# Performance work log

Hardware: AMD Instinct MI355X
Metric: run time of the kernel (lower is better)

The kernel has to match this reference:

```python
import jax, jax.numpy as jnp
import numpy as np

NUM_HEADS = 8
NUM_GROUPS = 32
EPS = 1e-4


def group_norm(x, scale, bias):
    # x: [b, L, C]; normalize over (L, channels-within-group) per flax GroupNorm
    b, l, c = x.shape
    xg = x.reshape(b, l, NUM_GROUPS, c // NUM_GROUPS)
    mean = jnp.mean(xg, axis=(1, 3), keepdims=True)
    var = jnp.var(xg, axis=(1, 3), keepdims=True)
    xg = (xg - mean) * jax.lax.rsqrt(var + EPS)
    return xg.reshape(b, l, c) * scale + bias


def setup_inputs() -> dict:
    key = jax.random.key(0)
    ks = jax.random.split(key, 6)
    bs, L, C = 4, 1024, 512
    hf = C // NUM_HEADS  # 64
    x = jax.random.normal(ks[0], (bs, L, C), dtype=jnp.float32)
    W_qkv = jax.random.normal(ks[1], (C, C * 2), dtype=jnp.float32) * (1.0 / C)
    gn_qkv_scale = jnp.ones((C * 2,), dtype=jnp.float32)
    gn_qkv_bias = jnp.zeros((C * 2,), dtype=jnp.float32)
    rel_emb = jax.random.normal(ks[2], (hf * 2, 2 * L - 1), dtype=jnp.float32) * (1.0 / hf)
    gn_out_scale = jnp.ones((C,), dtype=jnp.float32)
    gn_out_bias = jnp.zeros((C,), dtype=jnp.float32)
    return {
        "x": x,
        "W_qkv": W_qkv,
        "gn_qkv_scale": gn_qkv_scale,
        "gn_qkv_bias": gn_qkv_bias,
        "rel_emb": rel_emb,
        "gn_out_scale": gn_out_scale,
        "gn_out_bias": gn_out_bias,
    }


def reference(x, W_qkv, gn_qkv_scale, gn_qkv_bias, rel_emb, gn_out_scale, gn_out_bias):
    bs, L, C = x.shape
    hf = C // NUM_HEADS
    qkv = x @ W_qkv                                # [b, L, 2C]
    qkv = group_norm(qkv, gn_qkv_scale, gn_qkv_bias)
    qkv = qkv.reshape(bs, L, NUM_HEADS, hf * 2).transpose((0, 2, 3, 1))  # [b,h,2hf,L]
    q = qkv[:, :, : hf // 2]          # [b,h,hf/2,L]
    k = qkv[:, :, hf // 2: hf]        # [b,h,hf/2,L]
    v = qkv[:, :, hf:]                # [b,h,hf,L]
    # relative distance index: rel[i,j] = i - j + L - 1
    rel_idx = jnp.arange(L)[:, None] - jnp.arange(L)[None, :] + (L - 1)
    rpe = rel_emb[:, rel_idx]         # [2hf, L, L]
    rpe_q = rpe[: hf // 2]
    rpe_k = rpe[hf // 2: hf]
    rpe_v = rpe[hf:]
    logits = (
        jnp.einsum('bhdi,bhdj->bhij', q, k)
        + jnp.einsum('bhdi,dij->bhij', q, rpe_k)
        + jnp.einsum('bhdi,dij->bhij', k, rpe_q)
    )
    attn = jax.nn.softmax(logits, axis=3).astype(jnp.float32)
    wv = jnp.einsum('bhij,bhdj->bhdi', attn, v)
    wve = jnp.einsum('bhij,dij->bhdi', attn, rpe_v)
    out = (wv + wve).transpose((0, 3, 1, 2)).reshape(bs, L, C)
    return group_norm(out, gn_out_scale, gn_out_bias)
```

## Files before the change

### kernel.cpp

```cpp
#include <hip/hip_runtime.h>
#include <hip/hip_bf16.h>

typedef unsigned short ushort;
typedef __attribute__((ext_vector_type(8))) short bf16x8;
typedef __attribute__((ext_vector_type(4))) float f32x4;
typedef __attribute__((ext_vector_type(4))) unsigned short ushort4v;

#define BSZ  4
#define LSEQ 1024
#define CIN  512
#define C2   1024
#define NH   8
#define GEPS 1e-4f

static __device__ __forceinline__ ushort f2b(float f) {
    __hip_bfloat16 h = __float2bfloat16(f);
    return *reinterpret_cast<ushort*>(&h);
}
static __device__ __forceinline__ float b2f(ushort u) {
    __hip_bfloat16 h = *reinterpret_cast<__hip_bfloat16*>(&u);
    return __bfloat162float(h);
}

__global__ __launch_bounds__(256) void prep_xsplit(const float* __restrict__ x,
                                                   ushort* __restrict__ xh,
                                                   ushort* __restrict__ xl) {
    const size_t i4 = (size_t)blockIdx.x * 256 + threadIdx.x;
    const float4 v = *reinterpret_cast<const float4*>(&x[i4 * 4]);
    ushort4v h, lo;
    const float vv[4] = {v.x, v.y, v.z, v.w};
    #pragma unroll
    for (int c = 0; c < 4; ++c) {
        const ushort hh = f2b(vv[c]);
        h[c] = hh;
        lo[c] = f2b(vv[c] - b2f(hh));
    }
    *reinterpret_cast<ushort4v*>(&xh[i4 * 4]) = h;
    *reinterpret_cast<ushort4v*>(&xl[i4 * 4]) = lo;
}

__global__ __launch_bounds__(256) void prep_wT(const float* __restrict__ W,
                                               ushort* __restrict__ wth,
                                               ushort* __restrict__ wtl) {
    __shared__ float tl[64][65];
    const int k0 = blockIdx.y * 64, n0 = blockIdx.x * 64;
    const int t = threadIdx.x;
    #pragma unroll
    for (int u = 0; u < 16; ++u) {
        const int idx = t + 256 * u;
        const int kk = idx >> 6, nn = idx & 63;
        tl[kk][nn] = W[(size_t)(k0 + kk) * 1024 + n0 + nn];
    }
    __syncthreads();
    #pragma unroll
    for (int u = 0; u < 16; ++u) {
        const int idx = t + 256 * u;
        const int nn = idx >> 6, kk = idx & 63;
        const float v = tl[kk][nn];
        const ushort h = f2b(v);
        wth[(size_t)(n0 + nn) * 512 + k0 + kk] = h;
        wtl[(size_t)(n0 + nn) * 512 + k0 + kk] = f2b(v - b2f(h));
    }
}

__global__ __launch_bounds__(256) void prep_rel(const float* __restrict__ rel,
                                                ushort* __restrict__ relT,
                                                ushort* __restrict__ relV) {
    const int t = threadIdx.x;
    if (blockIdx.x < 32) {
        __shared__ float tl[64][65];
        const int r0 = blockIdx.x * 64;
        #pragma unroll
        for (int u = 0; u < 16; ++u) {
            const int idx = t + 256 * u;
            const int dd = idx >> 6, rr = idx & 63;
            int r = r0 + rr; if (r > 2046) r = 2046;
            tl[dd][rr] = rel[(size_t)(dd ^ 32) * 2047 + r];
        }
        __syncthreads();
        #pragma unroll
        for (int u = 0; u < 16; ++u) {
            const int idx = t + 256 * u;
            const int rr = idx >> 6, dd = idx & 63;
            relT[(size_t)(r0 + rr) * 64 + dd] = f2b(tl[dd][rr]);
        }
    } else {
        const int idx = (blockIdx.x - 32) * 256 + t;
        const int dv = idx >> 11, r = idx & 2047;
        const int rc = r > 2046 ? 2046 : r;
        relV[(size_t)dv * 2048 + r] = f2b(rel[(size_t)(64 + dv) * 2047 + rc]);
    }
}

__global__ __launch_bounds__(256) void gemm_qkv_mfma(const ushort* __restrict__ xh,
                                                     const ushort* __restrict__ xl,
                                                     const ushort* __restrict__ wth,
                                                     const ushort* __restrict__ wtl,
                                                     float* __restrict__ qkv,
                                                     float* __restrict__ sumq) {
    __shared__ ushort Ah[128][40];
    __shared__ ushort Al[128][40];
    __shared__ ushort Bh[128][40];
    __shared__ ushort Bl[128][40];
    const int t = threadIdx.x;
    const int w = t >> 6, l = t & 63;
    const int lr = l & 15, lq = l >> 4;
    const int wm = w >> 1, wn = w & 1;
    const int m0 = blockIdx.y * 128, n0 = blockIdx.x * 128;
    const int b = m0 >> 10;
    f32x4 acc[4][4] = {};
    for (int k0 = 0; k0 < 512; k0 += 32) {
        __syncthreads();
        #pragma unroll
        for (int u = 0; u < 2; ++u) {
            const int idx = t + 256 * u;
            const int r = idx >> 2, c16 = (idx & 3) * 8;
            *(bf16x8*)&Ah[r][c16] = *(const bf16x8*)&xh[(size_t)(m0 + r) * 512 + k0 + c16];
            *(bf16x8*)&Al[r][c16] = *(const bf16x8*)&xl[(size_t)(m0 + r) * 512 + k0 + c16];
            *(bf16x8*)&Bh[r][c16] = *(const bf16x8*)&wth[(size_t)(n0 + r) * 512 + k0 + c16];
            *(bf16x8*)&Bl[r][c16] = *(const bf16x8*)&wtl[(size_t)(n0 + r) * 512 + k0 + c16];
        }
        __syncthreads();
        bf16x8 ah[4], av[4];
        #pragma unroll
        for (int mi = 0; mi < 4; ++mi) {
            ah[mi] = *(const bf16x8*)&Ah[64 * wm + 16 * mi + lr][8 * lq];
            av[mi] = *(const bf16x8*)&Al[64 * wm + 16 * mi + lr][8 * lq];
        }
        #pragma unroll
        for (int ni = 0; ni < 4; ++ni) {
            const bf16x8 bh = *(const bf16x8*)&Bh[64 * wn + 16 * ni + lr][8 * lq];
            const bf16x8 bl = *(const bf16x8*)&Bl[64 * wn + 16 * ni + lr][8 * lq];
            #pragma unroll
            for (int mi = 0; mi < 4; ++mi) {
                f32x4 a = acc[mi][ni];
                a = __builtin_amdgcn_mfma_f32_16x16x32_bf16(ah[mi], bl, a, 0, 0, 0);
                a = __builtin_amdgcn_mfma_f32_16x16x32_bf16(av[mi], bh, a, 0, 0, 0);
                a = __builtin_amdgcn_mfma_f32_16x16x32_bf16(ah[mi], bh, a, 0, 0, 0);
                acc[mi][ni] = a;
            }
        }
    }
    #pragma unroll
    for (int mi = 0; mi < 4; ++mi)
        #pragma unroll
        for (int ni = 0; ni < 4; ++ni)
            #pragma unroll
            for (int e = 0; e < 4; ++e)
                qkv[(size_t)(m0 + 64 * wm + 16 * mi + 4 * lq + e) * 1024 + n0 + 64 * wn + 16 * ni + lr] = acc[mi][ni][e];
    #pragma unroll
    for (int ni = 0; ni < 4; ++ni) {
        float s = 0.f, s2 = 0.f;
        #pragma unroll
        for (int mi = 0; mi < 4; ++mi)
            #pragma unroll
            for (int e = 0; e < 4; ++e) { const float v = acc[mi][ni][e]; s += v; s2 += v * v; }
        #pragma unroll
        for (int o = 32; o; o >>= 1) { s += __shfl_xor(s, o, 64); s2 += __shfl_xor(s2, o, 64); }
        if (l == 0) {
            const int g = (n0 + 64 * wn + 16 * ni) >> 5;
            atomicAdd(&sumq[(b * 32 + g) * 2 + 0], s);
            atomicAdd(&sumq[(b * 32 + g) * 2 + 1], s2);
        }
    }
}

__global__ __launch_bounds__(256) void gn_apply_bf(const float* __restrict__ qkv,
                                                   const float* __restrict__ sumq,
                                                   const float* __restrict__ scale,
                                                   const float* __restrict__ bias,
                                                   ushort* __restrict__ qg,
                                                   ushort* __restrict__ qlo,
                                                   ushort* __restrict__ vb) {
    __shared__ float tile[64][65];
    const int b  = blockIdx.z;
    const int l0 = blockIdx.y * 64, c0 = blockIdx.x * 64;
    const int t  = threadIdx.x;
    const bool vhalf = (c0 & 64);
    const int h = c0 >> 7;
    #pragma unroll
    for (int u = 0; u < 16; ++u) {
        const int idx = t + 256 * u;
        const int lr = idx >> 6, cr = idx & 63;
        const int c = c0 + cr, g = c >> 5;
        const float s  = sumq[(b * 32 + g) * 2 + 0];
        const float s2 = sumq[(b * 32 + g) * 2 + 1];
        const float mu = s * (1.f / 32768.f);
        const float rr = rsqrtf(fmaxf(s2 * (1.f / 32768.f) - mu * mu, 0.f) + GEPS);
        float v = qkv[(size_t)(b * LSEQ + l0 + lr) * C2 + c];
        v = (v - mu) * rr * scale[c] + bias[c];
        const ushort hi = f2b(v);
        qg[(size_t)(b * LSEQ + l0 + lr) * C2 + c] = hi;
        if (vhalf) tile[lr][cr] = v;
        else qlo[(size_t)(b * LSEQ + l0 + lr) * 512 + h * 64 + cr] = f2b(v - b2f(hi));
    }
    if (vhalf) {
        __syncthreads();
        #pragma unroll
        for (int u = 0; u < 16; ++u) {
            const int idx = t + 256 * u;
            const int cw = idx >> 6, lw = idx & 63;
            vb[((size_t)((b * NH + h) * 64 + cw)) * LSEQ + l0 + lw] = f2b(tile[lw][cw]);
        }
    }
}

__global__ __launch_bounds__(256) void attn_mfma(const ushort* __restrict__ qg,
                                                 const ushort* __restrict__ qlo,
                                                 const ushort* __restrict__ vbuf,
                                                 const ushort* __restrict__ relT,
                                                 const ushort* __restrict__ relV,
                                                 float* __restrict__ aout,
                                                 float* __restrict__ sumo) {
    __shared__ __align__(16) ushort rT[128][72];
    __shared__ __align__(16) ushort rV[64][136];
    __shared__ __align__(16) ushort vj[64][72];
    __shared__ __align__(16) ushort TUb[4][16][88];
    __shared__ __align__(16) ushort Ps[4][16][72];
    __shared__ __align__(16) ushort Pr[4][16][104];

    const int t = threadIdx.x;
    const int w = t >> 6, l = t & 63;
    const int lr = l & 15, lq = l >> 4;
    const int i0 = blockIdx.x * 64;
    const int h = blockIdx.y, b = blockIdx.z;
    const int ck0 = w >> 1;

    const size_t arow = (size_t)(b * LSEQ + i0 + 16 * w + lr);
    const bf16x8 a_q  = *(const bf16x8*)&qg[arow * C2 + h * 128 + 8 * lq];
    const bf16x8 a_k  = *(const bf16x8*)&qg[arow * C2 + h * 128 + 32 + 8 * lq];
    const bf16x8 a_ql = *(const bf16x8*)&qlo[arow * 512 + h * 64 + 8 * lq];

    {
        uint* pz = (uint*)&Pr[w][0][0];
        #pragma unroll
        for (int u = 0; u < 13; ++u) pz[l + 64 * u] = 0;
    }

    float m_r[4], l_r[4];
    #pragma unroll
    for (int e = 0; e < 4; ++e) { m_r[e] = -3.0e38f; l_r[e] = 0.f; }
    f32x4 Oa[4] = {};

    const size_t vbase = (size_t)((b * NH + h) * 64) * LSEQ;
    const int tbase = 4 * lq + 63 - lr;
    const int prbase = 16 * w - 32 * ck0 + 63 + 4 * lq - lr;

    for (int j0 = 0; j0 < LSEQ; j0 += 64) {
        const int r0 = i0 - j0 + 960;
        __syncthreads();
        #pragma unroll
        for (int u = 0; u < 4; ++u) {
            const int idx = t + 256 * u;
            const int rl = idx >> 3, c8 = (idx & 7) * 8;
            *(bf16x8*)&rT[rl][c8] = *(const bf16x8*)&relT[(size_t)(r0 + rl) * 64 + c8];
        }
        #pragma unroll
        for (int u = 0; u < 4; ++u) {
            const int idx = t + 256 * u;
            const int dv = idx >> 4, c8 = (idx & 15) * 8;
            *(bf16x8*)&rV[dv][c8] = *(const bf16x8*)&relV[(size_t)dv * 2048 + r0 + c8];
        }
        #pragma unroll
        for (int u = 0; u < 2; ++u) {
            const int idx = t + 256 * u;
            const int dv = idx >> 3, c8 = (idx & 7) * 8;
            *(bf16x8*)&vj[dv][c8] = *(const bf16x8*)&vbuf[vbase + (size_t)dv * LSEQ + j0 + c8];
        }
        __syncthreads();

        #pragma unroll
        for (int ct5 = 0; ct5 < 5; ++ct5) {
            const int rr = 16 * (w + ct5) + lr;
            f32x4 acc = {0.f, 0.f, 0.f, 0.f};
            acc = __builtin_amdgcn_mfma_f32_16x16x32_bf16(a_q, *(const bf16x8*)&rT[rr][8 * lq], acc, 0, 0, 0);
            acc = __builtin_amdgcn_mfma_f32_16x16x32_bf16(a_k, *(const bf16x8*)&rT[rr][32 + 8 * lq], acc, 0, 0, 0);
            #pragma unroll
            for (int e = 0; e < 4; ++e) TUb[w][4 * lq + e][16 * ct5 + lr] = f2b(acc[e]);
        }

        f32x4 sv[4];
        #pragma unroll
        for (int n = 0; n < 4; ++n) {
            const size_t krow = (size_t)(b * LSEQ + j0 + 16 * n + lr);
            const bf16x8 b_hi = *(const bf16x8*)&qg[krow * C2 + h * 128 + 32 + 8 * lq];
            const bf16x8 b_lo = *(const bf16x8*)&qlo[krow * 512 + h * 64 + 32 + 8 * lq];
            f32x4 acc = {0.f, 0.f, 0.f, 0.f};
            acc = __builtin_amdgcn_mfma_f32_16x16x32_bf16(a_q,  b_lo, acc, 0, 0, 0);
            acc = __builtin_amdgcn_mfma_f32_16x16x32_bf16(a_ql, b_hi, acc, 0, 0, 0);
            acc = __builtin_amdgcn_mfma_f32_16x16x32_bf16(a_q,  b_hi, acc, 0, 0, 0);
            #pragma unroll
            for (int e = 0; e < 4; ++e) acc[e] += b2f(TUb[w][4 * lq + e][tbase + e - 16 * n]);
            sv[n] = acc;
        }

        float mx[4];
        #pragma unroll
        for (int e = 0; e < 4; ++e)
            mx[e] = fmaxf(fmaxf(sv[0][e], sv[1][e]), fmaxf(sv[2][e], sv[3][e]));
        #pragma unroll
        for (int o = 1; o < 16; o <<= 1)
            #pragma unroll
            for (int e = 0; e < 4; ++e) mx[e] = fmaxf(mx[e], __shfl_xor(mx[e], o, 64));
        float alpha[4], ssum[4];
        #pragma unroll
        for (int e = 0; e < 4; ++e) {
            const float mn = fmaxf(m_r[e], mx[e]);
            alpha[e] = __expf(m_r[e] - mn);
            m_r[e] = mn;
            ssum[e] = 0.f;
        }
        #pragma unroll
        for (int n = 0; n < 4; ++n)
            #pragma unroll
            for (int e = 0; e < 4; ++e) {
                const float p = __expf(sv[n][e] - m_r[e]);
                ssum[e] += p;
                const ushort pb = f2b(p);
                Ps[w][4 * lq + e][16 * n + lr] = pb;
                Pr[w][4 * lq + e][prbase + e - 16 * n] = pb;
            }
        #pragma unroll
        for (int o = 1; o < 16; o <<= 1)
            #pragma unroll
            for (int e = 0; e < 4; ++e) ssum[e] += __shfl_xor(ssum[e], o, 64);
        #pragma unroll
        for (int e = 0; e < 4; ++e) l_r[e] = l_r[e] * alpha[e] + ssum[e];

        const bf16x8 pa0 = *(const bf16x8*)&Ps[w][lr][8 * lq];
        const bf16x8 pa1 = *(const bf16x8*)&Ps[w][lr][32 + 8 * lq];
        bf16x8 pra[3];
        #pragma unroll
        for (int kk = 0; kk < 3; ++kk) pra[kk] = *(const bf16x8*)&Pr[w][lr][32 * kk + 8 * lq];
        #pragma unroll
        for (int n = 0; n < 4; ++n) {
            f32x4 acc = Oa[n];
            #pragma unroll
            for (int e = 0; e < 4; ++e) acc[e] *= alpha[e];
            acc = __builtin_amdgcn_mfma_f32_16x16x32_bf16(pa0, *(const bf16x8*)&vj[16 * n + lr][8 * lq], acc, 0, 0, 0);
            acc = __builtin_amdgcn_mfma_f32_16x16x32_bf16(pa1, *(const bf16x8*)&vj[16 * n + lr][32 + 8 * lq], acc, 0, 0, 0);
            #pragma unroll
            for (int kk = 0; kk < 3; ++kk) {
                const bf16x8 brv = *(const bf16x8*)&rV[16 * n + lr][32 * (ck0 + kk) + 8 * lq];
                acc = __builtin_amdgcn_mfma_f32_16x16x32_bf16(pra[kk], brv, acc, 0, 0, 0);
            }
            Oa[n] = acc;
        }
    }

    #pragma unroll
    for (int n = 0; n < 4; ++n) {
        float s = 0.f, s2 = 0.f;
        #pragma unroll
        for (int e = 0; e < 4; ++e) {
            const float o = Oa[n][e] / l_r[e];
            aout[((size_t)(b * LSEQ + i0 + 16 * w + 4 * lq + e)) * CIN + h * 64 + 16 * n + lr] = o;
            s += o; s2 += o * o;
        }
        #pragma unroll
        for (int o = 32; o; o >>= 1) { s += __shfl_xor(s, o, 64); s2 += __shfl_xor(s2, o, 64); }
        if (l == 0) {
            atomicAdd(&sumo[(b * 32 + h * 4 + n) * 2 + 0], s);
            atomicAdd(&sumo[(b * 32 + h * 4 + n) * 2 + 1], s2);
        }
    }
}

__global__ __launch_bounds__(256) void gn_out_apply(const float* __restrict__ aout,
                                                    const float* __restrict__ sumo,
                                                    const float* __restrict__ scale,
                                                    const float* __restrict__ bias,
                                                    float* __restrict__ out) {
    const int idx4 = blockIdx.x * 256 + threadIdx.x;
    const int c = (idx4 & 127) * 4;
    const size_t row = idx4 >> 7;
    const int b = (int)(row >> 10);
    const int g = c >> 4;
    const float s  = sumo[(b * 32 + g) * 2 + 0];
    const float s2 = sumo[(b * 32 + g) * 2 + 1];
    const float mu = s * (1.f / 16384.f);
    const float rr = rsqrtf(fmaxf(s2 * (1.f / 16384.f) - mu * mu, 0.f) + GEPS);
    const float4 v = *reinterpret_cast<const float4*>(&aout[row * 512 + c]);
    const float4 sc = *reinterpret_cast<const float4*>(&scale[c]);
    const float4 bi = *reinterpret_cast<const float4*>(&bias[c]);
    float4 o;
    o.x = (v.x - mu) * rr * sc.x + bi.x;
    o.y = (v.y - mu) * rr * sc.y + bi.y;
    o.z = (v.z - mu) * rr * sc.z + bi.z;
    o.w = (v.w - mu) * rr * sc.w + bi.w;
    *reinterpret_cast<float4*>(&out[row * 512 + c]) = o;
}

extern "C" void kernel_launch(void* const* d_in, const int* in_sizes, int n_in,
                              void* d_out, int out_size, void* d_ws, size_t ws_size,
                              hipStream_t stream) {
    (void)in_sizes; (void)n_in; (void)out_size; (void)ws_size;
    const float* x   = (const float*)d_in[0];
    const float* W   = (const float*)d_in[1];
    const float* gqs = (const float*)d_in[2];
    const float* gqb = (const float*)d_in[3];
    const float* rel = (const float*)d_in[4];
    const float* gos = (const float*)d_in[5];
    const float* gob = (const float*)d_in[6];
    float* out = (float*)d_out;

    char* ws = (char*)d_ws;
    float*  qkv  = (float*)ws;
    ushort* qg   = (ushort*)(ws + (16u << 20));
    ushort* vb   = (ushort*)(ws + (24u << 20));
    ushort* rTb  = (ushort*)(ws + (28u << 20));
    ushort* rVb  = (ushort*)(ws + (28u << 20) + (256u << 10));
    ushort* qlo  = (ushort*)(ws + (28u << 20) + (512u << 10));
    float*  aout = (float*)ws;
    float*  stats = (float*)(ws + (32u << 20) + (512u << 10));
    float* sumq = stats;
    float* sumo = stats + 256;
    ushort* xhi = (ushort*)(ws + (16u << 20));
    ushort* xlo = (ushort*)(ws + (20u << 20));
    ushort* wth = (ushort*)(ws + (24u << 20));
    ushort* wtl = (ushort*)(ws + (25u << 20));

    hipMemsetAsync(stats, 0, 2048, stream);
    prep_xsplit<<<2048, 256, 0, stream>>>(x, xhi, xlo);
    prep_wT<<<dim3(16, 8), 256, 0, stream>>>(W, wth, wtl);
    prep_rel<<<544, 256, 0, stream>>>(rel, rTb, rVb);
    gemm_qkv_mfma<<<dim3(8, 32), 256, 0, stream>>>(xhi, xlo, wth, wtl, qkv, sumq);
    gn_apply_bf<<<dim3(16, 16, BSZ), 256, 0, stream>>>(qkv, sumq, gqs, gqb, qg, qlo, vb);
    attn_mfma<<<dim3(16, NH, BSZ), 256, 0, stream>>>(qg, qlo, vb, rTb, rVb, aout, sumo);
    gn_out_apply<<<2048, 256, 0, stream>>>(aout, sumo, gos, gob, out);
}
```

Before: 231.9 us.

## Fuse prep kernels, use direct global-to-LDS loads with XOR swizzle, remap grids

Merges the three preprocessing kernels into one launch. The QKV GEMM and the attention kernel now load tiles with global_load_lds (16-byte direct-to-LDS) into unpadded, XOR-swizzled shared arrays. The GEMM tile shrinks to 128x64 so it launches 512 workgroups, and both kernels use a 1D grid with an XCD-aware block remap. The attention kernel also hoists the K operand loads ahead of the barrier and shares one LDS buffer between the TU and P stages. The aim is to cut launch overhead, VGPR staging of loads and LDS bank conflicts, and to raise occupancy and L2 locality, at the cost of more complex indexing.

```diff
diff --git a/kernel.cpp b/kernel.cpp
--- a/kernel.cpp
+++ b/kernel.cpp
@@ -2,6 +2,7 @@
 #include <hip/hip_bf16.h>
 
 typedef unsigned short ushort;
+typedef unsigned int uint;
 typedef __attribute__((ext_vector_type(8))) short bf16x8;
 typedef __attribute__((ext_vector_type(4))) float f32x4;
 typedef __attribute__((ext_vector_type(4))) unsigned short ushort4v;
@@ -22,73 +23,79 @@
     return __bfloat162float(h);
 }
 
-__global__ __launch_bounds__(256) void prep_xsplit(const float* __restrict__ x,
-                                                   ushort* __restrict__ xh,
-                                                   ushort* __restrict__ xl) {
-    const size_t i4 = (size_t)blockIdx.x * 256 + threadIdx.x;
-    const float4 v = *reinterpret_cast<const float4*>(&x[i4 * 4]);
-    ushort4v h, lo;
-    const float vv[4] = {v.x, v.y, v.z, v.w};
-    #pragma unroll
-    for (int c = 0; c < 4; ++c) {
-        const ushort hh = f2b(vv[c]);
-        h[c] = hh;
-        lo[c] = f2b(vv[c] - b2f(hh));
-    }
-    *reinterpret_cast<ushort4v*>(&xh[i4 * 4]) = h;
-    *reinterpret_cast<ushort4v*>(&xl[i4 * 4]) = lo;
-}
-
-__global__ __launch_bounds__(256) void prep_wT(const float* __restrict__ W,
-                                               ushort* __restrict__ wth,
-                                               ushort* __restrict__ wtl) {
-    __shared__ float tl[64][65];
-    const int k0 = blockIdx.y * 64, n0 = blockIdx.x * 64;
-    const int t = threadIdx.x;
-    #pragma unroll
-    for (int u = 0; u < 16; ++u) {
-        const int idx = t + 256 * u;
-        const int kk = idx >> 6, nn = idx & 63;
-        tl[kk][nn] = W[(size_t)(k0 + kk) * 1024 + n0 + nn];
-    }
-    __syncthreads();
-    #pragma unroll
-    for (int u = 0; u < 16; ++u) {
-        const int idx = t + 256 * u;
-        const int nn = idx >> 6, kk = idx & 63;
-        const float v = tl[kk][nn];
-        const ushort h = f2b(v);
-        wth[(size_t)(n0 + nn) * 512 + k0 + kk] = h;
-        wtl[(size_t)(n0 + nn) * 512 + k0 + kk] = f2b(v - b2f(h));
-    }
-}
-
-__global__ __launch_bounds__(256) void prep_rel(const float* __restrict__ rel,
+static __device__ __forceinline__ void gl16(const void* g, void* l) {
+    __builtin_amdgcn_global_load_lds((const __attribute__((address_space(1))) void*)g,
+                                     (__attribute__((address_space(3))) void*)l, 16, 0, 0);
+}
+
+__global__ __launch_bounds__(256) void prep_all(const float* __restrict__ x,
+                                                const float* __restrict__ W,
+                                                const float* __restrict__ rel,
+                                                ushort* __restrict__ xh,
+                                                ushort* __restrict__ xl,
+                                                ushort* __restrict__ wth,
+                                                ushort* __restrict__ wtl,
                                                 ushort* __restrict__ relT,
                                                 ushort* __restrict__ relV) {
+    __shared__ float tl[64][65];
     const int t = threadIdx.x;
-    if (blockIdx.x < 32) {
-        __shared__ float tl[64][65];
-        const int r0 = blockIdx.x * 64;
+    const int bid = blockIdx.x;
+    if (bid < 2048) {
+        const size_t i4 = (size_t)bid * 256 + t;
+        const float4 v = *reinterpret_cast<const float4*>(&x[i4 * 4]);
+        ushort4v h, lo;
+        const float vv[4] = {v.x, v.y, v.z, v.w};
+        #pragma unroll
+        for (int c = 0; c < 4; ++c) {
+            const ushort hh = f2b(vv[c]);
+            h[c] = hh;
+            lo[c] = f2b(vv[c] - b2f(hh));
+        }
+        *reinterpret_cast<ushort4v*>(&xh[i4 * 4]) = h;
+        *reinterpret_cast<ushort4v*>(&xl[i4 * 4]) = lo;
+    } else if (bid < 2176) {
+        const int bb = bid - 2048;
+        const int k0 = (bb >> 4) * 64, n0 = (bb & 15) * 64;
         #pragma unroll
         for (int u = 0; u < 16; ++u) {
             const int idx = t + 256 * u;
-            const int dd = idx >> 6, rr = idx & 63;
-            int r = r0 + rr; if (r > 2046) r = 2046;
-            tl[dd][rr] = rel[(size_t)(dd ^ 32) * 2047 + r];
+            const int kk = idx >> 6, nn = idx & 63;
+            tl[kk][nn] = W[(size_t)(k0 + kk) * 1024 + n0 + nn];
         }
         __syncthreads();
         #pragma unroll
         for (int u = 0; u < 16; ++u) {
             const int idx = t + 256 * u;
-            const int rr = idx >> 6, dd = idx & 63;
-            relT[(size_t)(r0 + rr) * 64 + dd] = f2b(tl[dd][rr]);
+            const int nn = idx >> 6, kk = idx & 63;
+            const float v = tl[kk][nn];
+            const ushort h = f2b(v);
+            wth[(size_t)(n0 + nn) * 512 + k0 + kk] = h;
+            wtl[(size_t)(n0 + nn) * 512 + k0 + kk] = f2b(v - b2f(h));
         }
     } else {
-        const int idx = (blockIdx.x - 32) * 256 + t;
-        const int dv = idx >> 11, r = idx & 2047;
-        const int rc = r > 2046 ? 2046 : r;
-        relV[(size_t)dv * 2048 + r] = f2b(rel[(size_t)(64 + dv) * 2047 + rc]);
+        const int bb = bid - 2176;
+        if (bb < 32) {
+            const int r0 = bb * 64;
+            #pragma unroll
+            for (int u = 0; u < 16; ++u) {
+                const int idx = t + 256 * u;
+                const int dd = idx >> 6, rr = idx & 63;
+                int r = r0 + rr; if (r > 2046) r = 2046;
+                tl[dd][rr] = rel[(size_t)(dd ^ 32) * 2047 + r];
+            }
+            __syncthreads();
+            #pragma unroll
+            for (int u = 0; u < 16; ++u) {
+                const int idx = t + 256 * u;
+                const int rr = idx >> 6, dd = idx & 63;
+                relT[(size_t)(r0 + rr) * 64 + dd] = f2b(tl[dd][rr]);
+            }
+        } else {
+            const int idx = (bb - 32) * 256 + t;
+            const int dv = idx >> 11, r = idx & 2047;
+            const int rc = r > 2046 ? 2046 : r;
+            relV[(size_t)dv * 2048 + r] = f2b(rel[(size_t)(64 + dv) * 2047 + rc]);
+        }
     }
 }
 
@@ -98,41 +105,55 @@
                                                      const ushort* __restrict__ wtl,
                                                      float* __restrict__ qkv,
                                                      float* __restrict__ sumq) {
-    __shared__ ushort Ah[128][40];
-    __shared__ ushort Al[128][40];
-    __shared__ ushort Bh[128][40];
-    __shared__ ushort Bl[128][40];
+    __shared__ ushort Ah[128][32];
+    __shared__ ushort Al[128][32];
+    __shared__ ushort Bh[64][32];
+    __shared__ ushort Bl[64][32];
     const int t = threadIdx.x;
     const int w = t >> 6, l = t & 63;
     const int lr = l & 15, lq = l >> 4;
-    const int wm = w >> 1, wn = w & 1;
-    const int m0 = blockIdx.y * 128, n0 = blockIdx.x * 128;
+    const int wg = blockIdx.x;
+    const int lg = (wg & 7) * 64 + (wg >> 3);
+    const int n0 = (lg & 15) * 64;
+    const int m0 = (lg >> 4) * 128;
     const int b = m0 >> 10;
-    f32x4 acc[4][4] = {};
+    f32x4 acc[2][4] = {};
     for (int k0 = 0; k0 < 512; k0 += 32) {
         __syncthreads();
         #pragma unroll
         for (int u = 0; u < 2; ++u) {
-            const int idx = t + 256 * u;
-            const int r = idx >> 2, c16 = (idx & 3) * 8;
-            *(bf16x8*)&Ah[r][c16] = *(const bf16x8*)&xh[(size_t)(m0 + r) * 512 + k0 + c16];
-            *(bf16x8*)&Al[r][c16] = *(const bf16x8*)&xl[(size_t)(m0 + r) * 512 + k0 + c16];
-            *(bf16x8*)&Bh[r][c16] = *(const bf16x8*)&wth[(size_t)(n0 + r) * 512 + k0 + c16];
-            *(bf16x8*)&Bl[r][c16] = *(const bf16x8*)&wtl[(size_t)(n0 + r) * 512 + k0 + c16];
-        }
-        __syncthreads();
-        bf16x8 ah[4], av[4];
-        #pragma unroll
-        for (int mi = 0; mi < 4; ++mi) {
-            ah[mi] = *(const bf16x8*)&Ah[64 * wm + 16 * mi + lr][8 * lq];
-            av[mi] = *(const bf16x8*)&Al[64 * wm + 16 * mi + lr][8 * lq];
+            const int s = (2 * w + u) * 64 + l;
+            const int row = s >> 2, pc = (s & 3) << 4;
+            const int lc = pc ^ ((row & 3) << 4);
+            const size_t src = (size_t)(m0 + row) * 512 + k0 + (lc >> 1);
+            gl16(&xh[src], (ushort*)&Ah[0][0] + (2 * w + u) * 512);
+            gl16(&xl[src], (ushort*)&Al[0][0] + (2 * w + u) * 512);
+        }
+        {
+            const int s = w * 64 + l;
+            const int row = s >> 2, pc = (s & 3) << 4;
+            const int lc = pc ^ ((row & 3) << 4);
+            const size_t src = (size_t)(n0 + row) * 512 + k0 + (lc >> 1);
+            gl16(&wth[src], (ushort*)&Bh[0][0] + w * 512);
+            gl16(&wtl[src], (ushort*)&Bl[0][0] + w * 512);
+        }
+        __syncthreads();
+        bf16x8 ah[2], av[2];
+        #pragma unroll
+        for (int mi = 0; mi < 2; ++mi) {
+            const int row = 32 * w + 16 * mi + lr;
+            const int sw = (row & 3) << 3;
+            ah[mi] = *(const bf16x8*)&Ah[row][(8 * lq) ^ sw];
+            av[mi] = *(const bf16x8*)&Al[row][(8 * lq) ^ sw];
         }
         #pragma unroll
         for (int ni = 0; ni < 4; ++ni) {
-            const bf16x8 bh = *(const bf16x8*)&Bh[64 * wn + 16 * ni + lr][8 * lq];
-            const bf16x8 bl = *(const bf16x8*)&Bl[64 * wn + 16 * ni + lr][8 * lq];
-            #pragma unroll
-            for (int mi = 0; mi < 4; ++mi) {
+            const int rowb = 16 * ni + lr;
+            const int swb = (rowb & 3) << 3;
+            const bf16x8 bh = *(const bf16x8*)&Bh[rowb][(8 * lq) ^ swb];
+            const bf16x8 bl = *(const bf16x8*)&Bl[rowb][(8 * lq) ^ swb];
+            #pragma unroll
+            for (int mi = 0; mi < 2; ++mi) {
                 f32x4 a = acc[mi][ni];
                 a = __builtin_amdgcn_mfma_f32_16x16x32_bf16(ah[mi], bl, a, 0, 0, 0);
                 a = __builtin_amdgcn_mfma_f32_16x16x32_bf16(av[mi], bh, a, 0, 0, 0);
@@ -142,23 +163,23 @@
         }
     }
     #pragma unroll
-    for (int mi = 0; mi < 4; ++mi)
+    for (int mi = 0; mi < 2; ++mi)
         #pragma unroll
         for (int ni = 0; ni < 4; ++ni)
             #pragma unroll
             for (int e = 0; e < 4; ++e)
-                qkv[(size_t)(m0 + 64 * wm + 16 * mi + 4 * lq + e) * 1024 + n0 + 64 * wn + 16 * ni + lr] = acc[mi][ni][e];
+                qkv[(size_t)(m0 + 32 * w + 16 * mi + 4 * lq + e) * 1024 + n0 + 16 * ni + lr] = acc[mi][ni][e];
     #pragma unroll
     for (int ni = 0; ni < 4; ++ni) {
         float s = 0.f, s2 = 0.f;
         #pragma unroll
-        for (int mi = 0; mi < 4; ++mi)
+        for (int mi = 0; mi < 2; ++mi)
             #pragma unroll
             for (int e = 0; e < 4; ++e) { const float v = acc[mi][ni][e]; s += v; s2 += v * v; }
         #pragma unroll
         for (int o = 32; o; o >>= 1) { s += __shfl_xor(s, o, 64); s2 += __shfl_xor(s2, o, 64); }
         if (l == 0) {
-            const int g = (n0 + 64 * wn + 16 * ni) >> 5;
+            const int g = (n0 + 16 * ni) >> 5;
             atomicAdd(&sumq[(b * 32 + g) * 2 + 0], s);
             atomicAdd(&sumq[(b * 32 + g) * 2 + 1], s2);
         }
@@ -212,18 +233,19 @@
                                                  const ushort* __restrict__ relV,
                                                  float* __restrict__ aout,
                                                  float* __restrict__ sumo) {
-    __shared__ __align__(16) ushort rT[128][72];
-    __shared__ __align__(16) ushort rV[64][136];
-    __shared__ __align__(16) ushort vj[64][72];
-    __shared__ __align__(16) ushort TUb[4][16][88];
-    __shared__ __align__(16) ushort Ps[4][16][72];
-    __shared__ __align__(16) ushort Pr[4][16][104];
+    __shared__ ushort rT[128][64];
+    __shared__ ushort rV[64][128];
+    __shared__ ushort vj[64][64];
+    __shared__ ushort sA[4][16][88];
+    __shared__ ushort sPr[4][16][104];
 
     const int t = threadIdx.x;
     const int w = t >> 6, l = t & 63;
     const int lr = l & 15, lq = l >> 4;
-    const int i0 = blockIdx.x * 64;
-    const int h = blockIdx.y, b = blockIdx.z;
+    const int wg = blockIdx.x;
+    const int lg = (wg & 7) * 64 + (wg >> 3);
+    const int ib = lg & 15, h = (lg >> 4) & 7, b = lg >> 7;
+    const int i0 = ib * 64;
     const int ck0 = w >> 1;
 
     const size_t arow = (size_t)(b * LSEQ + i0 + 16 * w + lr);
@@ -232,7 +254,7 @@
     const bf16x8 a_ql = *(const bf16x8*)&qlo[arow * 512 + h * 64 + 8 * lq];
 
     {
-        uint* pz = (uint*)&Pr[w][0][0];
+        uint* pz = (uint*)&sPr[w][0][0];
         #pragma unroll
         for (int u = 0; u < 13; ++u) pz[l + 64 * u] = 0;
     }
@@ -243,54 +265,64 @@
     f32x4 Oa[4] = {};
 
     const size_t vbase = (size_t)((b * NH + h) * 64) * LSEQ;
-    const int tbase = 4 * lq + 63 - lr;
+    const int tb = 4 * lq + 63 - lr;
     const int prbase = 16 * w - 32 * ck0 + 63 + 4 * lq - lr;
 
     for (int j0 = 0; j0 < LSEQ; j0 += 64) {
         const int r0 = i0 - j0 + 960;
+
+        bf16x8 kb_hi[4], kb_lo[4];
+        #pragma unroll
+        for (int n = 0; n < 4; ++n) {
+            const size_t krow = (size_t)(b * LSEQ + j0 + 16 * n + lr);
+            kb_hi[n] = *(const bf16x8*)&qg[krow * C2 + h * 128 + 32 + 8 * lq];
+            kb_lo[n] = *(const bf16x8*)&qlo[krow * 512 + h * 64 + 32 + 8 * lq];
+        }
+
         __syncthreads();
         #pragma unroll
         for (int u = 0; u < 4; ++u) {
-            const int idx = t + 256 * u;
-            const int rl = idx >> 3, c8 = (idx & 7) * 8;
-            *(bf16x8*)&rT[rl][c8] = *(const bf16x8*)&relT[(size_t)(r0 + rl) * 64 + c8];
+            const int s = (4 * w + u) * 64 + l;
+            const int row = s >> 3, pc = (s & 7) << 4;
+            const int lc = pc ^ ((row & 7) << 4);
+            gl16(&relT[(size_t)(r0 + row) * 64 + (lc >> 1)], (ushort*)&rT[0][0] + (4 * w + u) * 512);
         }
         #pragma unroll
         for (int u = 0; u < 4; ++u) {
-            const int idx = t + 256 * u;
-            const int dv = idx >> 4, c8 = (idx & 15) * 8;
-            *(bf16x8*)&rV[dv][c8] = *(const bf16x8*)&relV[(size_t)dv * 2048 + r0 + c8];
+            const int s = (4 * w + u) * 64 + l;
+            const int row = s >> 4, pc = (s & 15) << 4;
+            const int lc = pc ^ ((row & 7) << 4);
+            gl16(&relV[(size_t)row * 2048 + r0 + (lc >> 1)], (ushort*)&rV[0][0] + (4 * w + u) * 512);
         }
         #pragma unroll
         for (int u = 0; u < 2; ++u) {
-            const int idx = t + 256 * u;
-            const int dv = idx >> 3, c8 = (idx & 7) * 8;
-            *(bf16x8*)&vj[dv][c8] = *(const bf16x8*)&vbuf[vbase + (size_t)dv * LSEQ + j0 + c8];
+            const int s = (2 * w + u) * 64 + l;
+            const int row = s >> 3, pc = (s & 7) << 4;
+            const int lc = pc ^ ((row & 7) << 4);
+            gl16(&vbuf[vbase + (size_t)row * LSEQ + j0 + (lc >> 1)], (ushort*)&vj[0][0] + (2 * w + u) * 512);
         }
         __syncthreads();
 
         #pragma unroll
         for (int ct5 = 0; ct5 < 5; ++ct5) {
             const int rr = 16 * (w + ct5) + lr;
+            const int sw = (rr & 7) << 3;
             f32x4 acc = {0.f, 0.f, 0.f, 0.f};
-            acc = __builtin_amdgcn_mfma_f32_16x16x32_bf16(a_q, *(const bf16x8*)&rT[rr][8 * lq], acc, 0, 0, 0);
-            acc = __builtin_amdgcn_mfma_f32_16x16x32_bf16(a_k, *(const bf16x8*)&rT[rr][32 + 8 * lq], acc, 0, 0, 0);
-            #pragma unroll
-            for (int e = 0; e < 4; ++e) TUb[w][4 * lq + e][16 * ct5 + lr] = f2b(acc[e]);
+            acc = __builtin_amdgcn_mfma_f32_16x16x32_bf16(a_q, *(const bf16x8*)&rT[rr][(8 * lq) ^ sw], acc, 0, 0, 0);
+            acc = __builtin_amdgcn_mfma_f32_16x16x32_bf16(a_k, *(const bf16x8*)&rT[rr][(32 + 8 * lq) ^ sw], acc, 0, 0, 0);
+            #pragma unroll
+            for (int e = 0; e < 4; ++e) sA[w][4 * lq + e][16 * ct5 + lr] = f2b(acc[e]);
         }
 
         f32x4 sv[4];
         #pragma unroll
         for (int n = 0; n < 4; ++n) {
-            const size_t krow = (size_t)(b * LSEQ + j0 + 16 * n + lr);
-            const bf16x8 b_hi = *(const bf16x8*)&qg[krow * C2 + h * 128 + 32 + 8 * lq];
-            const bf16x8 b_lo = *(const bf16x8*)&qlo[krow * 512 + h * 64 + 32 + 8 * lq];
             f32x4 acc = {0.f, 0.f, 0.f, 0.f};
-            acc = __builtin_amdgcn_mfma_f32_16x16x32_bf16(a_q,  b_lo, acc, 0, 0, 0);
-            acc = __builtin_amdgcn_mfma_f32_16x16x32_bf16(a_ql, b_hi, acc, 0, 0, 0);
-            acc = __builtin_amdgcn_mfma_f32_16x16x32_bf16(a_q,  b_hi, acc, 0, 0, 0);
-            #pragma unroll
-            for (int e = 0; e < 4; ++e) acc[e] += b2f(TUb[w][4 * lq + e][tbase + e - 16 * n]);
+            acc = __builtin_amdgcn_mfma_f32_16x16x32_bf16(a_q,  kb_lo[n], acc, 0, 0, 0);
+            acc = __builtin_amdgcn_mfma_f32_16x16x32_bf16(a_ql, kb_hi[n], acc, 0, 0, 0);
+            acc = __builtin_amdgcn_mfma_f32_16x16x32_bf16(a_q,  kb_hi[n], acc, 0, 0, 0);
+            #pragma unroll
+            for (int e = 0; e < 4; ++e) acc[e] += b2f(sA[w][4 * lq + e][tb + e - 16 * n]);
             sv[n] = acc;
         }
 
@@ -317,8 +349,8 @@
                 const float p = __expf(sv[n][e] - m_r[e]);
                 ssum[e] += p;
                 const ushort pb = f2b(p);
-                Ps[w][4 * lq + e][16 * n + lr] = pb;
-                Pr[w][4 * lq + e][prbase + e - 16 * n] = pb;
+                sA[w][4 * lq + e][16 * n + lr] = pb;
+                sPr[w][4 * lq + e][prbase + e - 16 * n] = pb;
             }
         #pragma unroll
         for (int o = 1; o < 16; o <<= 1)
@@ -327,22 +359,24 @@
         #pragma unroll
         for (int e = 0; e < 4; ++e) l_r[e] = l_r[e] * alpha[e] + ssum[e];
 
-        const bf16x8 pa0 = *(const bf16x8*)&Ps[w][lr][8 * lq];
-        const bf16x8 pa1 = *(const bf16x8*)&Ps[w][lr][32 + 8 * lq];
+        const bf16x8 pa0 = *(const bf16x8*)&sA[w][lr][8 * lq];
+        const bf16x8 pa1 = *(const bf16x8*)&sA[w][lr][32 + 8 * lq];
         bf16x8 pra[3];
         #pragma unroll
-        for (int kk = 0; kk < 3; ++kk) pra[kk] = *(const bf16x8*)&Pr[w][lr][32 * kk + 8 * lq];
+        for (int kk = 0; kk < 3; ++kk) pra[kk] = *(const bf16x8*)&sPr[w][lr][32 * kk + 8 * lq];
         #pragma unroll
         for (int n = 0; n < 4; ++n) {
+            const int rw = 16 * n + lr;
+            const int sw = (rw & 7) << 3;
             f32x4 acc = Oa[n];
             #pragma unroll
             for (int e = 0; e < 4; ++e) acc[e] *= alpha[e];
-            acc = __builtin_amdgcn_mfma_f32_16x16x32_bf16(pa0, *(const bf16x8*)&vj[16 * n + lr][8 * lq], acc, 0, 0, 0);
-            acc = __builtin_amdgcn_mfma_f32_16x16x32_bf16(pa1, *(const bf16x8*)&vj[16 * n + lr][32 + 8 * lq], acc, 0, 0, 0);
+            acc = __builtin_amdgcn_mfma_f32_16x16x32_bf16(pa0, *(const bf16x8*)&vj[rw][(8 * lq) ^ sw], acc, 0, 0, 0);
+            acc = __builtin_amdgcn_mfma_f32_16x16x32_bf16(pa1, *(const bf16x8*)&vj[rw][(32 + 8 * lq) ^ sw], acc, 0, 0, 0);
             #pragma unroll
             for (int kk = 0; kk < 3; ++kk) {
-                const bf16x8 brv = *(const bf16x8*)&rV[16 * n + lr][32 * (ck0 + kk) + 8 * lq];
-                acc = __builtin_amdgcn_mfma_f32_16x16x32_bf16(pra[kk], brv, acc, 0, 0, 0);
+                acc = __builtin_amdgcn_mfma_f32_16x16x32_bf16(pra[kk],
+                        *(const bf16x8*)&rV[rw][(32 * (ck0 + kk) + 8 * lq) ^ sw], acc, 0, 0, 0);
             }
             Oa[n] = acc;
         }
@@ -421,11 +455,9 @@
     ushort* wtl = (ushort*)(ws + (25u << 20));
 
     hipMemsetAsync(stats, 0, 2048, stream);
-    prep_xsplit<<<2048, 256, 0, stream>>>(x, xhi, xlo);
-    prep_wT<<<dim3(16, 8), 256, 0, stream>>>(W, wth, wtl);
-    prep_rel<<<544, 256, 0, stream>>>(rel, rTb, rVb);
-    gemm_qkv_mfma<<<dim3(8, 32), 256, 0, stream>>>(xhi, xlo, wth, wtl, qkv, sumq);
+    prep_all<<<2720, 256, 0, stream>>>(x, W, rel, xhi, xlo, wth, wtl, rTb, rVb);
+    gemm_qkv_mfma<<<512, 256, 0, stream>>>(xhi, xlo, wth, wtl, qkv, sumq);
     gn_apply_bf<<<dim3(16, 16, BSZ), 256, 0, stream>>>(qkv, sumq, gqs, gqb, qg, qlo, vb);
-    attn_mfma<<<dim3(16, NH, BSZ), 256, 0, stream>>>(qg, qlo, vb, rTb, rVb, aout, sumo);
+    attn_mfma<<<512, 256, 0, stream>>>(qg, qlo, vb, rTb, rVb, aout, sumo);
     gn_out_apply<<<2048, 256, 0, stream>>>(aout, sumo, gos, gob, out);
 }
```

Measured after the change: 230.6 us. Within noise of the previous version (-0.5%).
